# Kernel tuning notes

Measured on AMD Instinct MI355X. Metric: run time of the kernel, lower is better.

The kernel has to match this reference:

```python
import jax, jax.numpy as jnp
import numpy as np

D_MODEL = 512
NUM_HEADS = 8
D_K = D_MODEL // NUM_HEADS


def setup_inputs() -> dict:
    key = jax.random.key(0)
    k0, k1, k2, k3, k4 = jax.random.split(key, 5)
    s = 1.0 / np.sqrt(D_MODEL)
    return {
        "x": jax.random.normal(k0, (2, 4096, D_MODEL), dtype=jnp.float32),
        "W_q": jax.random.normal(k1, (D_MODEL, D_MODEL), dtype=jnp.float32) * s,
        "W_k": jax.random.normal(k2, (D_MODEL, D_MODEL), dtype=jnp.float32) * s,
        "W_v": jax.random.normal(k3, (D_MODEL, D_MODEL), dtype=jnp.float32) * s,
        "W_o": jax.random.normal(k4, (D_MODEL, D_MODEL), dtype=jnp.float32) * s,
    }


def reference(x, W_q, W_k, W_v, W_o):
    B, S, _ = x.shape
    # project and split heads: (B, H, S, d_k)
    def split(t):
        return t.reshape(B, S, NUM_HEADS, D_K).transpose(0, 2, 1, 3)
    Q = split(x @ W_q)
    K = split(x @ W_k)
    V = split(x @ W_v)
    scale = jnp.sqrt(jnp.asarray(D_K, dtype=x.dtype))
    logits = jnp.einsum('bhqd,bhkd->bhqk', Q, K) / scale
    attn = jax.nn.softmax(logits, axis=-1)  # dropout is identity at inference
    out = jnp.einsum('bhqk,bhkd->bhqd', attn, V)
    concat = out.transpose(0, 2, 1, 3).reshape(B, S, D_MODEL)
    return concat @ W_o
```

## Files before the change

kernel.cpp:

```cpp
#include <hip/hip_runtime.h>
#include <hip/hip_bf16.h>


#define DMODEL 512
#define SEQ    4096
#define NTOK   8192
#define LDQK   1024

#define LGKM_BARRIER() do { \
  asm volatile("s_waitcnt lgkmcnt(0)" ::: "memory"); \
  __builtin_amdgcn_s_barrier(); \
} while (0)

using f32x4 = __attribute__((ext_vector_type(4))) float;
using s16x8 = __attribute__((ext_vector_type(8))) short;
using u16x8 = __attribute__((ext_vector_type(8))) unsigned short;

static __device__ __forceinline__ unsigned short f2bf(float f) {
  union { float f; unsigned u; } v; v.f = f;
  unsigned r = v.u + 0x7fff + ((v.u >> 16) & 1);
  return (unsigned short)(r >> 16);
}

static __device__ __forceinline__ unsigned pack_bf2(float lo, float hi) {
  __hip_bfloat162 t = __float22bfloat162_rn(make_float2(lo, hi));
  union { __hip_bfloat162 b; unsigned u; } c; c.b = t; return c.u;
}

static __device__ __forceinline__ void gll16(const void* g, void* l) {
  __builtin_amdgcn_global_load_lds(
      (const __attribute__((address_space(1))) unsigned int*)g,
      (__attribute__((address_space(3))) unsigned int*)l, 16, 0, 0);
}

__global__ void prep_kernel(const float* __restrict__ x,
                            const float* __restrict__ Wq,
                            const float* __restrict__ Wk,
                            const float* __restrict__ Wv,
                            const float* __restrict__ Wo,
                            unsigned short* __restrict__ xb,
                            unsigned short* __restrict__ Wall, float c2) {
  __shared__ float T[64][65];
  const int bx = blockIdx.x;
  if (bx < 1024) {
    for (int i = bx * 256 + threadIdx.x; i < NTOK * DMODEL / 4; i += 262144) {
      float4 v = ((const float4*)x)[i];
      ushort4 o;
      o.x = f2bf(v.x); o.y = f2bf(v.y); o.z = f2bf(v.z); o.w = f2bf(v.w);
      ((ushort4*)xb)[i] = o;
    }
    return;
  }
  const int t = bx - 1024;
  const int y = t >> 6, sub = t & 63;
  const float* W = (y == 0) ? Wq : (y == 1) ? Wk : (y == 2) ? Wv : Wo;
  const float scale = (y == 0) ? c2 : 1.0f;
  const int tk = (sub & 7) * 64;
  const int tn = (sub >> 3) * 64;
  const int r  = threadIdx.x >> 2;
  const int cq = threadIdx.x & 3;
#pragma unroll
  for (int i = 0; i < 4; ++i) {
    int c = (cq + 4 * i) * 4;
    float4 v = *(const float4*)&W[(size_t)(tk + r) * 512 + tn + c];
    T[r][c + 0] = v.x * scale; T[r][c + 1] = v.y * scale;
    T[r][c + 2] = v.z * scale; T[r][c + 3] = v.w * scale;
  }
  __syncthreads();
  const int n  = threadIdx.x >> 2;
  const int k0 = (threadIdx.x & 3) * 16;
#pragma unroll
  for (int j4 = 0; j4 < 4; ++j4) {
    ushort4 o;
    o.x = f2bf(T[k0 + j4 * 4 + 0][n]);
    o.y = f2bf(T[k0 + j4 * 4 + 1][n]);
    o.z = f2bf(T[k0 + j4 * 4 + 2][n]);
    o.w = f2bf(T[k0 + j4 * 4 + 3][n]);
    *(ushort4*)&Wall[(size_t)y * 262144 + (size_t)(tn + n) * 512 + tk + k0 + j4 * 4] = o;
  }
}

__global__ __launch_bounds__(256, 3) void gemm_qkv(
    const unsigned short* __restrict__ xb,
    const unsigned short* __restrict__ Wall,
    unsigned short* __restrict__ QKb,
    unsigned short* __restrict__ Vtb)
{
  __shared__ unsigned short As[128 * 64];
  __shared__ unsigned short Bs[128 * 64];
  const int by = blockIdx.y;
  const bool vmode = (by >= 8);
  const unsigned short* A  = vmode ? (Wall + 2 * 262144) : xb;
  const unsigned short* Bt = vmode ? xb : Wall;
  const size_t bm = vmode ? (size_t)(by - 8) * 128 : (size_t)blockIdx.x * 128;
  const size_t bn = vmode ? (size_t)blockIdx.x * 128 : (size_t)by * 128;
  const int tid  = threadIdx.x;
  const int wave = tid >> 6, lane = tid & 63;
  const int q4 = lane >> 4, ln = lane & 15;
  const int wm = (wave >> 1) * 64, wn = (wave & 1) * 64;
  f32x4 acc[4][4] = {};

  const int rlo  = lane >> 3;
  const int sbx  = ((lane & 7) << 4) ^ (rlo << 4);
  const int rswz = (ln & 7) << 4;

  const char* Asb = (const char*)A  + (size_t)(bm + wave * 32 + rlo) * 1024 + sbx;
  const char* Bsb = (const char*)Bt + (size_t)(bn + wave * 32 + rlo) * 1024 + sbx;
  char* Adst = (char*)As + wave * 4096;
  char* Bdst = (char*)Bs + wave * 4096;

  for (int kt = 0; kt < 512; kt += 64) {
    __syncthreads();
#pragma unroll
    for (int j = 0; j < 4; ++j) {
      gll16(Asb + kt * 2 + j * 8192, Adst + j * 1024);
      gll16(Bsb + kt * 2 + j * 8192, Bdst + j * 1024);
    }
    __syncthreads();
    s16x8 bfr[4][2];
#pragma unroll
    for (int ni = 0; ni < 4; ni++) {
      const char* bb = (char*)Bs + (wn + ni * 16 + ln) * 128;
      bfr[ni][0] = *(const s16x8*)(bb + ((q4 * 16)      ^ rswz));
      bfr[ni][1] = *(const s16x8*)(bb + ((q4 * 16 + 64) ^ rswz));
    }
#pragma unroll
    for (int mi = 0; mi < 4; mi++) {
      const char* ab = (char*)As + (wm + mi * 16 + ln) * 128;
      s16x8 af0 = *(const s16x8*)(ab + ((q4 * 16)      ^ rswz));
      s16x8 af1 = *(const s16x8*)(ab + ((q4 * 16 + 64) ^ rswz));
#pragma unroll
      for (int ni = 0; ni < 4; ni++) {
        acc[mi][ni] = __builtin_amdgcn_mfma_f32_16x16x32_bf16(
            af0, bfr[ni][0], acc[mi][ni], 0, 0, 0);
        acc[mi][ni] = __builtin_amdgcn_mfma_f32_16x16x32_bf16(
            af1, bfr[ni][1], acc[mi][ni], 0, 0, 0);
      }
    }
  }
#pragma unroll
  for (int mi = 0; mi < 4; mi++)
#pragma unroll
    for (int r = 0; r < 4; ++r) {
      size_t row = bm + wm + mi * 16 + q4 * 4 + r;
#pragma unroll
      for (int ni = 0; ni < 4; ni++) {
        size_t col = bn + wn + ni * 16 + ln;
        unsigned short hv = f2bf(acc[mi][ni][r]);
        if (!vmode) {
          QKb[row * 1024 + col] = hv;
        } else {
          int b = (int)(col >> 12), s = (int)(col & 4095);
          int sp = (s & ~63) | (s & 32) | (((s >> 2) & 3) << 3) |
                   (((s >> 4) & 1) << 2) | (s & 3);
          Vtb[(size_t)b * 2097152 + row * 4096 + sp] = hv;
        }
      }
    }
}

__global__ __launch_bounds__(256, 2) void attn_kernel(
    const unsigned short* __restrict__ QK,
    const unsigned short* __restrict__ Vt,
    unsigned short* __restrict__ Oc)
{
  const int bid = blockIdx.x + 32 * (blockIdx.y + 8 * blockIdx.z);
  const int lin = (bid & 7) * 64 + (bid >> 3);
  const int qt = lin & 31, bh = lin >> 5;
  const int h = bh & 7, b = bh >> 3;
  const int tid = threadIdx.x, wave = tid >> 6, lane = tid & 63;
  const int q4 = lane >> 4, ln = lane & 15;
  __shared__ unsigned short Ks[2][64 * 64];
  __shared__ unsigned short Vs[2][64 * 64];
  const size_t rowbase = (size_t)b * SEQ;
  const size_t qrow0   = (size_t)qt * 128 + wave * 32;
  const unsigned short* Kp  = QK + rowbase * LDQK + 512 + h * 64;
  const unsigned short* VTp = Vt + ((size_t)(b * 8 + h) * 64) * SEQ;

  s16x8 qf[2][2];
#pragma unroll
  for (int mf = 0; mf < 2; ++mf) {
    const unsigned short* q = QK + (rowbase + qrow0 + mf * 16 + ln) * LDQK + h * 64;
    qf[mf][0] = *(const s16x8*)(q + q4 * 8);
    qf[mf][1] = *(const s16x8*)(q + 32 + q4 * 8);
  }
  f32x4 o[2][4] = {};
  f32x4 ol[2]   = {};
  s16x8 onesf;
#pragma unroll
  for (int j = 0; j < 8; ++j) onesf[j] = (short)0x3F80;

  const int srow = tid >> 2;
  const int c32  = (tid & 3) * 32;
  const int swz  = (srow & 7) << 4;
  const int wof0 = srow * 128 + ((c32 +  0) ^ swz);
  const int wof1 = srow * 128 + ((c32 + 16) ^ swz);
  const int rswz = (ln & 7) << 4;

  const unsigned short* kgp = Kp  + (size_t)srow * LDQK + (c32 >> 1);
  const unsigned short* vgp = VTp + (size_t)srow * SEQ + (c32 >> 1);

  u16x8 kr  = *(const u16x8*)kgp;
  u16x8 kr2 = *(const u16x8*)(kgp + 8);
  u16x8 vr  = *(const u16x8*)vgp;
  u16x8 vr2 = *(const u16x8*)(vgp + 8);
  *(u16x8*)((char*)Ks[0] + wof0) = kr;
  *(u16x8*)((char*)Ks[0] + wof1) = kr2;
  *(u16x8*)((char*)Vs[0] + wof0) = vr;
  *(u16x8*)((char*)Vs[0] + wof1) = vr2;
  kgp += (size_t)64 * LDQK;  vgp += 64;
  kr  = *(const u16x8*)kgp;
  kr2 = *(const u16x8*)(kgp + 8);
  vr  = *(const u16x8*)vgp;
  vr2 = *(const u16x8*)(vgp + 8);
  LGKM_BARRIER();

  const f32x4 fz = {0.f, 0.f, 0.f, 0.f};

  s16x8 vfp[2][4];
  s16x8 pfp[2][2];

  {
    const char* Kc = (const char*)Ks[0];
    const char* Vc = (const char*)Vs[0];
    f32x4 s4[2][4];
#pragma unroll
    for (int ni = 0; ni < 4; ni++) {
      const char* kb = Kc + (ni * 16 + ln) * 128;
      s16x8 kf0 = *(const s16x8*)(kb + ((q4 * 16)      ^ rswz));
      s16x8 kf1 = *(const s16x8*)(kb + ((q4 * 16 + 64) ^ rswz));
      __builtin_amdgcn_s_setprio(1);
#pragma unroll
      for (int mf = 0; mf < 2; ++mf) {
        f32x4 acc0 = __builtin_amdgcn_mfma_f32_16x16x32_bf16(kf0, qf[mf][0], fz, 0, 0, 0);
        s4[mf][ni] = __builtin_amdgcn_mfma_f32_16x16x32_bf16(kf1, qf[mf][1], acc0, 0, 0, 0);
      }
      __builtin_amdgcn_s_setprio(0);
    }
#pragma unroll
    for (int ks = 0; ks < 2; ++ks)
#pragma unroll
      for (int ni = 0; ni < 4; ni++)
        vfp[ks][ni] = *(const s16x8*)(Vc + (ni * 16 + ln) * 128 +
                                      ((ks * 64 + q4 * 16) ^ rswz));
#pragma unroll
    for (int mf = 0; mf < 2; ++mf) {
      float e[4][4];
#pragma unroll
      for (int ni = 0; ni < 4; ni++)
#pragma unroll
        for (int r = 0; r < 4; ++r)
          e[ni][r] = __builtin_amdgcn_exp2f(s4[mf][ni][r]);
#pragma unroll
      for (int ks = 0; ks < 2; ++ks) {
        union { s16x8 v; unsigned u[4]; } pu;
        pu.u[0] = pack_bf2(e[2 * ks][0],     e[2 * ks][1]);
        pu.u[1] = pack_bf2(e[2 * ks][2],     e[2 * ks][3]);
        pu.u[2] = pack_bf2(e[2 * ks + 1][0], e[2 * ks + 1][1]);
        pu.u[3] = pack_bf2(e[2 * ks + 1][2], e[2 * ks + 1][3]);
        pfp[mf][ks] = pu.v;
      }
    }
    char* Kn = (char*)Ks[1];
    char* Vn = (char*)Vs[1];
    *(u16x8*)(Kn + wof0) = kr;
    *(u16x8*)(Kn + wof1) = kr2;
    *(u16x8*)(Vn + wof0) = vr;
    *(u16x8*)(Vn + wof1) = vr2;
    kgp += (size_t)64 * LDQK;  vgp += 64;
    kr  = *(const u16x8*)kgp;
    kr2 = *(const u16x8*)(kgp + 8);
    vr  = *(const u16x8*)vgp;
    vr2 = *(const u16x8*)(vgp + 8);
    LGKM_BARRIER();
  }

#pragma unroll 2
  for (int t = 1; t < 64; ++t) {
    const int cur = t & 1;
    const char* Kc = (const char*)Ks[cur];
    const char* Vc = (const char*)Vs[cur];

    f32x4 s4[2][4];
#pragma unroll
    for (int ni = 0; ni < 4; ni++) {
      const char* kb = Kc + (ni * 16 + ln) * 128;
      s16x8 kf0 = *(const s16x8*)(kb + ((q4 * 16)      ^ rswz));
      s16x8 kf1 = *(const s16x8*)(kb + ((q4 * 16 + 64) ^ rswz));
      __builtin_amdgcn_s_setprio(1);
#pragma unroll
      for (int mf = 0; mf < 2; ++mf) {
        f32x4 acc0 = __builtin_amdgcn_mfma_f32_16x16x32_bf16(kf0, qf[mf][0], fz, 0, 0, 0);
        s4[mf][ni] = __builtin_amdgcn_mfma_f32_16x16x32_bf16(kf1, qf[mf][1], acc0, 0, 0, 0);
      }
      __builtin_amdgcn_s_setprio(0);
    }

#pragma unroll
    for (int ks = 0; ks < 2; ++ks)
#pragma unroll
      for (int ni = 0; ni < 4; ni++)
#pragma unroll
        for (int mf = 0; mf < 2; ++mf)
          o[mf][ni] = __builtin_amdgcn_mfma_f32_16x16x32_bf16(pfp[mf][ks], vfp[ks][ni], o[mf][ni], 0, 0, 0);
#pragma unroll
    for (int mf = 0; mf < 2; ++mf)
#pragma unroll
      for (int ks = 0; ks < 2; ++ks)
        ol[mf] = __builtin_amdgcn_mfma_f32_16x16x32_bf16(pfp[mf][ks], onesf, ol[mf], 0, 0, 0);

    s16x8 vfc[2][4];
#pragma unroll
    for (int ks = 0; ks < 2; ++ks)
#pragma unroll
      for (int ni = 0; ni < 4; ni++)
        vfc[ks][ni] = *(const s16x8*)(Vc + (ni * 16 + ln) * 128 +
                                      ((ks * 64 + q4 * 16) ^ rswz));

    s16x8 pfc[2][2];
#pragma unroll
    for (int mf = 0; mf < 2; ++mf) {
      float e[4][4];
#pragma unroll
      for (int ni = 0; ni < 4; ni++)
#pragma unroll
        for (int r = 0; r < 4; ++r)
          e[ni][r] = __builtin_amdgcn_exp2f(s4[mf][ni][r]);
#pragma unroll
      for (int ks = 0; ks < 2; ++ks) {
        union { s16x8 v; unsigned u[4]; } pu;
        pu.u[0] = pack_bf2(e[2 * ks][0],     e[2 * ks][1]);
        pu.u[1] = pack_bf2(e[2 * ks][2],     e[2 * ks][3]);
        pu.u[2] = pack_bf2(e[2 * ks + 1][0], e[2 * ks + 1][1]);
        pu.u[3] = pack_bf2(e[2 * ks + 1][2], e[2 * ks + 1][3]);
        pfc[mf][ks] = pu.v;
      }
    }

    if (t + 1 < 64) {
      char* Kn = (char*)Ks[cur ^ 1];
      char* Vn = (char*)Vs[cur ^ 1];
      *(u16x8*)(Kn + wof0) = kr;
      *(u16x8*)(Kn + wof1) = kr2;
      *(u16x8*)(Vn + wof0) = vr;
      *(u16x8*)(Vn + wof1) = vr2;
      if (t + 2 < 64) {
        kgp += (size_t)64 * LDQK;  vgp += 64;
        kr  = *(const u16x8*)kgp;
        kr2 = *(const u16x8*)(kgp + 8);
        vr  = *(const u16x8*)vgp;
        vr2 = *(const u16x8*)(vgp + 8);
      }
    }

#pragma unroll
    for (int ks = 0; ks < 2; ++ks)
#pragma unroll
      for (int ni = 0; ni < 4; ni++)
        vfp[ks][ni] = vfc[ks][ni];
#pragma unroll
    for (int mf = 0; mf < 2; ++mf)
#pragma unroll
      for (int ks = 0; ks < 2; ++ks)
        pfp[mf][ks] = pfc[mf][ks];

    LGKM_BARRIER();
  }

  __builtin_amdgcn_s_setprio(1);
#pragma unroll
  for (int ks = 0; ks < 2; ++ks)
#pragma unroll
    for (int ni = 0; ni < 4; ni++)
#pragma unroll
      for (int mf = 0; mf < 2; ++mf)
        o[mf][ni] = __builtin_amdgcn_mfma_f32_16x16x32_bf16(pfp[mf][ks], vfp[ks][ni], o[mf][ni], 0, 0, 0);
#pragma unroll
  for (int mf = 0; mf < 2; ++mf)
#pragma unroll
    for (int ks = 0; ks < 2; ++ks)
      ol[mf] = __builtin_amdgcn_mfma_f32_16x16x32_bf16(pfp[mf][ks], onesf, ol[mf], 0, 0, 0);
  __builtin_amdgcn_s_setprio(0);

#pragma unroll
  for (int mf = 0; mf < 2; ++mf)
#pragma unroll
    for (int r = 0; r < 4; ++r) {
      const float nv = 1.0f / ol[mf][r];
      const size_t row = rowbase + qrow0 + mf * 16 + q4 * 4 + r;
#pragma unroll
      for (int ni = 0; ni < 4; ni++)
        Oc[row * 512 + h * 64 + ni * 16 + ln] = f2bf(o[mf][ni][r] * nv);
    }
}

__global__ __launch_bounds__(256, 3) void gemm_out(
    const unsigned short* __restrict__ A,
    const unsigned short* __restrict__ Bt,
    float* __restrict__ C)
{
  __shared__ unsigned short As[128 * 64];
  __shared__ unsigned short Bs[64 * 64];
  const int tid  = threadIdx.x;
  const int wave = tid >> 6, lane = tid & 63;
  const int q4 = lane >> 4, ln = lane & 15;
  const size_t bm = (size_t)blockIdx.x * 128;
  const size_t bn = (size_t)blockIdx.y * 64;
  const int wm = (wave >> 1) * 64, wn = (wave & 1) * 32;
  f32x4 acc[4][2] = {};

  const int rlo  = lane >> 3;
  const int sbx  = ((lane & 7) << 4) ^ (rlo << 4);
  const int rswz = (ln & 7) << 4;

  const char* Asb = (const char*)A  + (size_t)(bm + wave * 32 + rlo) * 1024 + sbx;
  const char* Bsb = (const char*)Bt + (size_t)(bn + wave * 16 + rlo) * 1024 + sbx;
  char* Adst = (char*)As + wave * 4096;
  char* Bdst = (char*)Bs + wave * 2048;

  for (int kt = 0; kt < 512; kt += 64) {
    __syncthreads();
#pragma unroll
    for (int j = 0; j < 4; ++j)
      gll16(Asb + kt * 2 + j * 8192, Adst + j * 1024);
#pragma unroll
    for (int j = 0; j < 2; ++j)
      gll16(Bsb + kt * 2 + j * 8192, Bdst + j * 1024);
    __syncthreads();
    s16x8 bfr[2][2];
#pragma unroll
    for (int ni = 0; ni < 2; ni++) {
      const char* bb = (char*)Bs + (wn + ni * 16 + ln) * 128;
      bfr[ni][0] = *(const s16x8*)(bb + ((q4 * 16)      ^ rswz));
      bfr[ni][1] = *(const s16x8*)(bb + ((q4 * 16 + 64) ^ rswz));
    }
#pragma unroll
    for (int mi = 0; mi < 4; mi++) {
      const char* ab = (char*)As + (wm + mi * 16 + ln) * 128;
      s16x8 af0 = *(const s16x8*)(ab + ((q4 * 16)      ^ rswz));
      s16x8 af1 = *(const s16x8*)(ab + ((q4 * 16 + 64) ^ rswz));
#pragma unroll
      for (int ni = 0; ni < 2; ni++) {
        acc[mi][ni] = __builtin_amdgcn_mfma_f32_16x16x32_bf16(
            af0, bfr[ni][0], acc[mi][ni], 0, 0, 0);
        acc[mi][ni] = __builtin_amdgcn_mfma_f32_16x16x32_bf16(
            af1, bfr[ni][1], acc[mi][ni], 0, 0, 0);
      }
    }
  }
#pragma unroll
  for (int mi = 0; mi < 4; mi++)
#pragma unroll
    for (int r = 0; r < 4; ++r) {
      size_t row = bm + wm + mi * 16 + q4 * 4 + r;
#pragma unroll
      for (int ni = 0; ni < 2; ni++)
        C[row * 512 + bn + wn + ni * 16 + ln] = acc[mi][ni][r];
    }
}

extern "C" void kernel_launch(void* const* d_in, const int* in_sizes, int n_in,
                              void* d_out, int out_size, void* d_ws, size_t ws_size,
                              hipStream_t stream) {
  const float* x  = (const float*)d_in[0];
  const float* Wq = (const float*)d_in[1];
  const float* Wk = (const float*)d_in[2];
  const float* Wv = (const float*)d_in[3];
  const float* Wo = (const float*)d_in[4];

  char* ws = (char*)d_ws;
  unsigned short* xb    = (unsigned short*)(ws);
  unsigned short* Wall  = (unsigned short*)(ws + 8388608);
  unsigned short* QKb   = (unsigned short*)(ws + 10485760);
  unsigned short* Vtb   = (unsigned short*)(ws + 27262976);
  unsigned short* Oc    = (unsigned short*)(ws + 35651584);

  const float C2 = 0.125f * 1.44269504088896f;

  hipLaunchKernelGGL(prep_kernel, dim3(1280), dim3(256), 0, stream,
                     x, Wq, Wk, Wv, Wo, xb, Wall, C2);
  hipLaunchKernelGGL(gemm_qkv, dim3(64, 12), dim3(256), 0, stream,
                     xb, Wall, QKb, Vtb);
  hipLaunchKernelGGL(attn_kernel, dim3(32, 8, 2), dim3(256), 0, stream,
                     QKb, Vtb, Oc);
  hipLaunchKernelGGL(gemm_out, dim3(64, 8), dim3(256), 0, stream,
                     Oc, Wall + 3 * 262144, (float*)d_out);
}
```

Baseline: 185.0 us.

## Load K and V fragments directly from global memory, dropping LDS staging

The attention kernel no longer stages K and V tiles in double-buffered shared memory behind a barrier. Each wave now loads its MFMA operand fragments straight from global memory into registers, prefetching the next K tile one iteration ahead. This removes the LDS writes, the swizzled LDS reads and the per-iteration workgroup barrier. In exchange, every wave re-reads the same K/V data from global memory or cache, and V is loaded with no prefetch distance, so latency may be exposed.

```diff
diff --git a/kernel.cpp b/kernel.cpp
--- a/kernel.cpp
+++ b/kernel.cpp
@@ -6,11 +6,6 @@
 #define SEQ    4096
 #define NTOK   8192
 #define LDQK   1024
-
-#define LGKM_BARRIER() do { \
-  asm volatile("s_waitcnt lgkmcnt(0)" ::: "memory"); \
-  __builtin_amdgcn_s_barrier(); \
-} while (0)
 
 using f32x4 = __attribute__((ext_vector_type(4))) float;
 using s16x8 = __attribute__((ext_vector_type(8))) short;
@@ -170,8 +165,6 @@
   const int h = bh & 7, b = bh >> 3;
   const int tid = threadIdx.x, wave = tid >> 6, lane = tid & 63;
   const int q4 = lane >> 4, ln = lane & 15;
-  __shared__ unsigned short Ks[2][64 * 64];
-  __shared__ unsigned short Vs[2][64 * 64];
   const size_t rowbase = (size_t)b * SEQ;
   const size_t qrow0   = (size_t)qt * 128 + wave * 32;
   const unsigned short* Kp  = QK + rowbase * LDQK + 512 + h * 64;
@@ -190,59 +183,44 @@
 #pragma unroll
   for (int j = 0; j < 8; ++j) onesf[j] = (short)0x3F80;
 
-  const int srow = tid >> 2;
-  const int c32  = (tid & 3) * 32;
-  const int swz  = (srow & 7) << 4;
-  const int wof0 = srow * 128 + ((c32 +  0) ^ swz);
-  const int wof1 = srow * 128 + ((c32 + 16) ^ swz);
-  const int rswz = (ln & 7) << 4;
-
-  const unsigned short* kgp = Kp  + (size_t)srow * LDQK + (c32 >> 1);
-  const unsigned short* vgp = VTp + (size_t)srow * SEQ + (c32 >> 1);
-
-  u16x8 kr  = *(const u16x8*)kgp;
-  u16x8 kr2 = *(const u16x8*)(kgp + 8);
-  u16x8 vr  = *(const u16x8*)vgp;
-  u16x8 vr2 = *(const u16x8*)(vgp + 8);
-  *(u16x8*)((char*)Ks[0] + wof0) = kr;
-  *(u16x8*)((char*)Ks[0] + wof1) = kr2;
-  *(u16x8*)((char*)Vs[0] + wof0) = vr;
-  *(u16x8*)((char*)Vs[0] + wof1) = vr2;
-  kgp += (size_t)64 * LDQK;  vgp += 64;
-  kr  = *(const u16x8*)kgp;
-  kr2 = *(const u16x8*)(kgp + 8);
-  vr  = *(const u16x8*)vgp;
-  vr2 = *(const u16x8*)(vgp + 8);
-  LGKM_BARRIER();
+  const unsigned short* kkp = Kp  + (size_t)ln * LDQK + q4 * 8;
+  const unsigned short* vvp = VTp + (size_t)ln * SEQ  + q4 * 8;
+
+  s16x8 kfn[4][2];
+  auto load_k = [&](int t) {
+#pragma unroll
+    for (int ni = 0; ni < 4; ni++) {
+      const unsigned short* p = kkp + ((size_t)t * 64 + ni * 16) * LDQK;
+      kfn[ni][0] = *(const s16x8*)p;
+      kfn[ni][1] = *(const s16x8*)(p + 32);
+    }
+  };
 
   const f32x4 fz = {0.f, 0.f, 0.f, 0.f};
 
   s16x8 vfp[2][4];
   s16x8 pfp[2][2];
 
+  load_k(0);
+
   {
-    const char* Kc = (const char*)Ks[0];
-    const char* Vc = (const char*)Vs[0];
     f32x4 s4[2][4];
 #pragma unroll
     for (int ni = 0; ni < 4; ni++) {
-      const char* kb = Kc + (ni * 16 + ln) * 128;
-      s16x8 kf0 = *(const s16x8*)(kb + ((q4 * 16)      ^ rswz));
-      s16x8 kf1 = *(const s16x8*)(kb + ((q4 * 16 + 64) ^ rswz));
       __builtin_amdgcn_s_setprio(1);
 #pragma unroll
       for (int mf = 0; mf < 2; ++mf) {
-        f32x4 acc0 = __builtin_amdgcn_mfma_f32_16x16x32_bf16(kf0, qf[mf][0], fz, 0, 0, 0);
-        s4[mf][ni] = __builtin_amdgcn_mfma_f32_16x16x32_bf16(kf1, qf[mf][1], acc0, 0, 0, 0);
+        f32x4 acc0 = __builtin_amdgcn_mfma_f32_16x16x32_bf16(kfn[ni][0], qf[mf][0], fz, 0, 0, 0);
+        s4[mf][ni] = __builtin_amdgcn_mfma_f32_16x16x32_bf16(kfn[ni][1], qf[mf][1], acc0, 0, 0, 0);
       }
       __builtin_amdgcn_s_setprio(0);
     }
+    load_k(1);
 #pragma unroll
     for (int ks = 0; ks < 2; ++ks)
 #pragma unroll
       for (int ni = 0; ni < 4; ni++)
-        vfp[ks][ni] = *(const s16x8*)(Vc + (ni * 16 + ln) * 128 +
-                                      ((ks * 64 + q4 * 16) ^ rswz));
+        vfp[ks][ni] = *(const s16x8*)(vvp + (size_t)(ni * 16) * SEQ + ks * 32);
 #pragma unroll
     for (int mf = 0; mf < 2; ++mf) {
       float e[4][4];
@@ -261,40 +239,23 @@
         pfp[mf][ks] = pu.v;
       }
     }
-    char* Kn = (char*)Ks[1];
-    char* Vn = (char*)Vs[1];
-    *(u16x8*)(Kn + wof0) = kr;
-    *(u16x8*)(Kn + wof1) = kr2;
-    *(u16x8*)(Vn + wof0) = vr;
-    *(u16x8*)(Vn + wof1) = vr2;
-    kgp += (size_t)64 * LDQK;  vgp += 64;
-    kr  = *(const u16x8*)kgp;
-    kr2 = *(const u16x8*)(kgp + 8);
-    vr  = *(const u16x8*)vgp;
-    vr2 = *(const u16x8*)(vgp + 8);
-    LGKM_BARRIER();
   }
 
 #pragma unroll 2
   for (int t = 1; t < 64; ++t) {
-    const int cur = t & 1;
-    const char* Kc = (const char*)Ks[cur];
-    const char* Vc = (const char*)Vs[cur];
-
     f32x4 s4[2][4];
 #pragma unroll
     for (int ni = 0; ni < 4; ni++) {
-      const char* kb = Kc + (ni * 16 + ln) * 128;
-      s16x8 kf0 = *(const s16x8*)(kb + ((q4 * 16)      ^ rswz));
-      s16x8 kf1 = *(const s16x8*)(kb + ((q4 * 16 + 64) ^ rswz));
       __builtin_amdgcn_s_setprio(1);
 #pragma unroll
       for (int mf = 0; mf < 2; ++mf) {
-        f32x4 acc0 = __builtin_amdgcn_mfma_f32_16x16x32_bf16(kf0, qf[mf][0], fz, 0, 0, 0);
-        s4[mf][ni] = __builtin_amdgcn_mfma_f32_16x16x32_bf16(kf1, qf[mf][1], acc0, 0, 0, 0);
+        f32x4 acc0 = __builtin_amdgcn_mfma_f32_16x16x32_bf16(kfn[ni][0], qf[mf][0], fz, 0, 0, 0);
+        s4[mf][ni] = __builtin_amdgcn_mfma_f32_16x16x32_bf16(kfn[ni][1], qf[mf][1], acc0, 0, 0, 0);
       }
       __builtin_amdgcn_s_setprio(0);
     }
+
+    if (t + 1 < 64) load_k(t + 1);
 
 #pragma unroll
     for (int ks = 0; ks < 2; ++ks)
@@ -314,8 +275,8 @@
     for (int ks = 0; ks < 2; ++ks)
 #pragma unroll
       for (int ni = 0; ni < 4; ni++)
-        vfc[ks][ni] = *(const s16x8*)(Vc + (ni * 16 + ln) * 128 +
-                                      ((ks * 64 + q4 * 16) ^ rswz));
+        vfc[ks][ni] = *(const s16x8*)(vvp + (size_t)(ni * 16) * SEQ +
+                                      (size_t)t * 64 + ks * 32);
 
     s16x8 pfc[2][2];
 #pragma unroll
@@ -337,22 +298,6 @@
       }
     }
 
-    if (t + 1 < 64) {
-      char* Kn = (char*)Ks[cur ^ 1];
-      char* Vn = (char*)Vs[cur ^ 1];
-      *(u16x8*)(Kn + wof0) = kr;
-      *(u16x8*)(Kn + wof1) = kr2;
-      *(u16x8*)(Vn + wof0) = vr;
-      *(u16x8*)(Vn + wof1) = vr2;
-      if (t + 2 < 64) {
-        kgp += (size_t)64 * LDQK;  vgp += 64;
-        kr  = *(const u16x8*)kgp;
-        kr2 = *(const u16x8*)(kgp + 8);
-        vr  = *(const u16x8*)vgp;
-        vr2 = *(const u16x8*)(vgp + 8);
-      }
-    }
-
 #pragma unroll
     for (int ks = 0; ks < 2; ++ks)
 #pragma unroll
@@ -363,8 +308,6 @@
 #pragma unroll
       for (int ks = 0; ks < 2; ++ks)
         pfp[mf][ks] = pfc[mf][ks];
-
-    LGKM_BARRIER();
   }
 
   __builtin_amdgcn_s_setprio(1);
```

Measured after the change: 336.3 us. +81.8%, slower.
